# Performance work log

Measured on AMD Instinct MI355X. Metric: run time of the kernel, lower is better.

## Reference

```python
import jax, jax.numpy as jnp
import numpy as np

# Problem constants (from config / init_kwargs)
B = 32768          # batch_size
T = 20             # T_observation
N = 4              # N_agents
D = 8              # state_dim
H = 64             # gru_hidden_size


def setup_inputs() -> dict:
    key = jax.random.key(0)
    ks = jax.random.split(key, 6)
    s = lambda fan_in: 1.0 / np.sqrt(fan_in)
    return {
        "x": jax.random.normal(ks[0], (B, T * N * D), dtype=jnp.float32),
        # per-agent GRU weights: input proj (no bias), hidden proj (with bias); 3H = r|z|n
        "Wi": jax.random.normal(ks[1], (N, D, 3 * H), dtype=jnp.float32) * s(D),
        "Wh": jax.random.normal(ks[2], (N, H, 3 * H), dtype=jnp.float32) * s(H),
        "bh": jnp.zeros((N, 3 * H), dtype=jnp.float32),
        # MLP head: 256 -> 256 -> 128 -> 8
        "W0": jax.random.normal(ks[3], (N * H, 256), dtype=jnp.float32) * s(N * H),
        "b0": jnp.zeros((256,), dtype=jnp.float32),
        "W1": jax.random.normal(ks[4], (256, 128), dtype=jnp.float32) * s(256),
        "b1": jnp.zeros((128,), dtype=jnp.float32),
        "Wout": jax.random.normal(ks[5], (128, 8), dtype=jnp.float32) * s(128),
        "bout": jnp.zeros((8,), dtype=jnp.float32),
    }


def reference(x, Wi, Wh, bh, W0, b0, W1, b1, Wout, bout):
    b = x.shape[0]
    xr = x.reshape(b, T, N, D)
    # Precompute input-side gate projections for all agents/timesteps at once.
    xi = jnp.einsum("btnd,ndk->tbnk", xr, Wi)  # [T, B, N, 3H]

    def step(h, xi_t):
        # h: [B, N, H]; xi_t: [B, N, 3H]
        hg = jnp.einsum("bnh,nhk->bnk", h, Wh) + bh  # [B, N, 3H]
        ir, iz, inn = jnp.split(xi_t, 3, axis=-1)
        hr, hz, hn = jnp.split(hg, 3, axis=-1)
        r = jax.nn.sigmoid(ir + hr)
        z = jax.nn.sigmoid(iz + hz)
        n = jnp.tanh(inn + r * hn)
        h_new = (1.0 - z) * n + z * h  # flax GRUCell update
        return h_new, None

    h0 = jnp.zeros((b, N, H), dtype=x.dtype)
    hT, _ = jax.lax.scan(step, h0, xi)
    feat = hT.reshape(b, N * H)  # concat per-agent final hidden states

    h1 = jax.nn.relu(feat @ W0 + b0)
    h2 = jax.nn.relu(h1 @ W1 + b1)  # dropout deterministic -> identity
    goals = h2 @ Wout + bout
    return goals
```

## Files before the change

### kernel.cpp

```cpp
#include <hip/hip_runtime.h>
#include <math.h>

#define BT 32768
#define TT 20
#define NA 4
#define DD 8
#define HH 64

typedef _Float16 half8 __attribute__((ext_vector_type(8)));
typedef float f32x4 __attribute__((ext_vector_type(4)));
typedef unsigned short ushort;
typedef unsigned int uint;

#define SC1 -1.4426950408889634f
#define SC2 -2.8853900817779268f

__device__ __forceinline__ ushort f16b(float v) {
    _Float16 h = (_Float16)v;
    return *(ushort*)&h;
}
__device__ __forceinline__ void fsplit(float v, ushort& hi, ushort& lo) {
    _Float16 h = (_Float16)v;
    hi = *(ushort*)&h;
    float r = v - (float)h;
    _Float16 lw = (_Float16)r;
    lo = *(ushort*)&lw;
}

__global__ void prep_all(const float* __restrict__ Wh, const float* __restrict__ Wi,
                         const float* __restrict__ bh, const float* __restrict__ W0,
                         const float* __restrict__ W1, const float* __restrict__ Wout,
                         uint4* __restrict__ AG, uint4* __restrict__ W0F,
                         uint4* __restrict__ W1F, uint4* __restrict__ W2F) {
    const int gid = blockIdx.x * 256 + threadIdx.x;
    if (gid < 20480) {
        const int l = gid & 63;
        const int r2 = gid >> 6;
        const int fid = r2 % 20;
        const int jt = (r2 / 20) & 3;
        const int n = r2 / 80;
        const int s = fid & 1;
        const int gk = fid >> 1;
        int g, kq;
        if (gk < 9) { g = gk / 3; kq = gk % 3; } else { g = 3; kq = 2; }
        const int j = jt * 16 + (l & 15);
        const int lk = (l >> 4) & 3;
        const float scale = (g < 2) ? SC1 : SC2;
        uint wds[4];
        for (int i = 0; i < 4; ++i) {
            uint pk = 0;
            for (int hf = 0; hf < 2; ++hf) {
                const int e = 2 * i + hf;
                const int k = kq * 32 + 8 * lk + e;
                float v = 0.f;
                if (g < 3) {
                    if (k < 64)       v = Wh[(size_t)(n * 64 + k) * 192 + g * 64 + j];
                    else if (k < 72)  { if (g < 2) v = Wi[(size_t)(n * 8 + (k - 64)) * 192 + g * 64 + j]; }
                    else if (k == 72) v = bh[n * 192 + g * 64 + j];
                } else {
                    if (k >= 64 && k < 72) v = Wi[(size_t)(n * 8 + (k - 64)) * 192 + 128 + j];
                }
                v *= scale;
                ushort hi, lo; fsplit(v, hi, lo);
                pk |= ((uint)(s ? lo : hi)) << (16 * hf);
            }
            wds[i] = pk;
        }
        uint4 u; u.x = wds[0]; u.y = wds[1]; u.z = wds[2]; u.w = wds[3];
        AG[gid] = u;
    } else if (gid < 33024) {
        int id; const float* W; uint4* dst; int Nreal;
        if (gid < 28672)      { id = gid - 20480; W = W0;   dst = W0F; Nreal = 256; }
        else if (gid < 32768) { id = gid - 28672; W = W1;   dst = W1F; Nreal = 128; }
        else                  { id = gid - 32768; W = Wout; dst = W2F; Nreal = 8;   }
        const int l = id & 63;
        const int rr = id >> 6;
        const int kq = rr & 7;
        const int nt = rr >> 3;
        const int o = nt * 16 + (l & 15);
        const int lk = (l >> 4) & 3;
        const int ocols = (Nreal < 16) ? Nreal : ((Nreal + 15) & ~15);
        uint wds[4];
        for (int i = 0; i < 4; ++i) {
            uint pk = 0;
            for (int hf = 0; hf < 2; ++hf) {
                const int e = 2 * i + hf;
                const int k = kq * 32 + 8 * lk + e;
                float v = 0.f;
                if (o < Nreal) v = W[(size_t)k * Nreal + o];
                pk |= ((uint)f16b(v)) << (16 * hf);
            }
            wds[i] = pk;
        }
        uint4 u; u.x = wds[0]; u.y = wds[1]; u.z = wds[2]; u.w = wds[3];
        dst[id] = u;
        (void)ocols;
    }
}

__global__ __launch_bounds__(256, 2)
void gru_kernel(const float* __restrict__ x, const uint4* __restrict__ AG,
                ushort* __restrict__ featH, ushort* __restrict__ featL) {
    __shared__ __align__(16) ushort Bs[2][2][32 * 128];
    const int tid = threadIdx.x;
    const int l = tid & 63;
    const int w = tid >> 6;
    const int lrow = l & 15;
    const int lk = l >> 4;
    const int jt2 = w >> 1;
    const int nt = w & 1;
    const int n = blockIdx.y;
    const int bg = blockIdx.x * 32;

    {
        uint4 z = {0, 0, 0, 0};
        uint4* p = (uint4*)&Bs[0][0][0];
        for (int i = tid; i < 2048; i += 256) p[i] = z;
    }
    __syncthreads();

    half8 A[2][20];
#pragma unroll
    for (int jl = 0; jl < 2; ++jl) {
        const uint4* __restrict__ ab = AG + (size_t)((n * 4 + (jt2 * 2 + jl)) * 20) * 64 + l;
#pragma unroll
        for (int f = 0; f < 20; ++f) {
            uint4 v = ab[f * 64];
            A[jl][f] = *(half8*)&v;
        }
    }

    const int m0 = tid >> 3, d0 = tid & 7;
    const float* __restrict__ xp = x + (size_t)(bg + m0) * 640 + n * 8 + d0;

    {
        float v = xp[0];
        ushort hi, lo; fsplit(v, hi, lo);
        const int gsw = 8 ^ (m0 & 7);
        Bs[0][0][m0 * 128 + gsw * 8 + d0] = hi;
        Bs[0][1][m0 * 128 + gsw * 8 + d0] = lo;
    }
    if (tid < 64) {
        const int m = tid & 31, bu = tid >> 5;
        Bs[bu][0][m * 128 + (9 ^ (m & 7)) * 8 + 0] = 0x3C00;
    }
    __syncthreads();

    f32x4 hold[2];
#pragma unroll
    for (int jl = 0; jl < 2; ++jl)
#pragma unroll
        for (int r = 0; r < 4; ++r) hold[jl][r] = 0.f;

    const int rbase = (nt * 16 + lrow) * 128;
    const int key = lrow & 7;

    for (int t = 0; t < TT; ++t) {
        const int p = t & 1;
        float xnext = 0.f;
        if (t < TT - 1) xnext = xp[(t + 1) * 32];

        const ushort* __restrict__ BH = &Bs[p][0][0];
        const ushort* __restrict__ BL = &Bs[p][1][0];
        ushort* __restrict__ WH = &Bs[p ^ 1][0][0];
        ushort* __restrict__ WL = &Bs[p ^ 1][1][0];

        f32x4 acc[2][4];
#pragma unroll
        for (int jl = 0; jl < 2; ++jl)
#pragma unroll
            for (int g = 0; g < 4; ++g)
#pragma unroll
                for (int r = 0; r < 4; ++r) acc[jl][g][r] = 0.f;

#pragma unroll
        for (int kq = 0; kq < 3; ++kq) {
            const int gsw = (kq * 4 + lk) ^ key;
            const half8 bhf = *(const half8*)&BH[rbase + gsw * 8];
            const half8 blf = *(const half8*)&BL[rbase + gsw * 8];
#pragma unroll
            for (int jl = 0; jl < 2; ++jl) {
#pragma unroll
                for (int g = 0; g < 3; ++g) {
                    acc[jl][g] = __builtin_amdgcn_mfma_f32_16x16x32_f16(A[jl][(g * 3 + kq) * 2 + 0], bhf, acc[jl][g], 0, 0, 0);
                    acc[jl][g] = __builtin_amdgcn_mfma_f32_16x16x32_f16(A[jl][(g * 3 + kq) * 2 + 1], bhf, acc[jl][g], 0, 0, 0);
                    acc[jl][g] = __builtin_amdgcn_mfma_f32_16x16x32_f16(A[jl][(g * 3 + kq) * 2 + 0], blf, acc[jl][g], 0, 0, 0);
                }
                if (kq == 2) {
                    acc[jl][3] = __builtin_amdgcn_mfma_f32_16x16x32_f16(A[jl][18], bhf, acc[jl][3], 0, 0, 0);
                    acc[jl][3] = __builtin_amdgcn_mfma_f32_16x16x32_f16(A[jl][19], bhf, acc[jl][3], 0, 0, 0);
                    acc[jl][3] = __builtin_amdgcn_mfma_f32_16x16x32_f16(A[jl][18], blf, acc[jl][3], 0, 0, 0);
                }
            }
        }

#pragma unroll
        for (int jl = 0; jl < 2; ++jl) {
            float hv[4];
#pragma unroll
            for (int r = 0; r < 4; ++r) {
                const float rg = __builtin_amdgcn_rcpf(1.f + __builtin_amdgcn_exp2f(acc[jl][0][r]));
                const float zg = __builtin_amdgcn_rcpf(1.f + __builtin_amdgcn_exp2f(acc[jl][1][r]));
                const float sarg = fmaf(rg, acc[jl][2][r], acc[jl][3][r]);
                const float sg = __builtin_amdgcn_rcpf(1.f + __builtin_amdgcn_exp2f(sarg));
                const float ng = fmaf(2.f, sg, -1.f);
                hv[r] = fmaf(zg, hold[jl][r] - ng, ng);
                hold[jl][r] = hv[r];
            }
            if (t < TT - 1) {
                ushort hh[4], hl[4];
#pragma unroll
                for (int r = 0; r < 4; ++r) fsplit(hv[r], hh[r], hl[r]);
                const int jtg = jt2 * 2 + jl;
                const int gsw = (2 * jtg + (lk >> 1)) ^ key;
                const int off = rbase + gsw * 8 + 4 * (lk & 1);
                uint2 ph, pl;
                ph.x = (uint)hh[0] | ((uint)hh[1] << 16);
                ph.y = (uint)hh[2] | ((uint)hh[3] << 16);
                pl.x = (uint)hl[0] | ((uint)hl[1] << 16);
                pl.y = (uint)hl[2] | ((uint)hl[3] << 16);
                *(uint2*)&WH[off] = ph;
                *(uint2*)&WL[off] = pl;
            }
        }
        if (t < TT - 1) {
            ushort hi, lo; fsplit(xnext, hi, lo);
            const int gsw = 8 ^ (m0 & 7);
            WH[m0 * 128 + gsw * 8 + d0] = hi;
            WL[m0 * 128 + gsw * 8 + d0] = lo;
        }
        __syncthreads();
    }

#pragma unroll
    for (int jl = 0; jl < 2; ++jl) {
        ushort fh[4], fl[4];
#pragma unroll
        for (int r = 0; r < 4; ++r) fsplit(hold[jl][r], fh[r], fl[r]);
        uint2 ph, pl;
        ph.x = (uint)fh[0] | ((uint)fh[1] << 16);
        ph.y = (uint)fh[2] | ((uint)fh[3] << 16);
        pl.x = (uint)fl[0] | ((uint)fl[1] << 16);
        pl.y = (uint)fl[2] | ((uint)fl[3] << 16);
        const size_t fo = (size_t)(bg + nt * 16 + lrow) * 256 + n * 64 + (jt2 * 2 + jl) * 16 + 4 * lk;
        *(uint2*)&featH[fo] = ph;
        *(uint2*)&featL[fo] = pl;
    }
}

__global__ __launch_bounds__(256, 3)
void mlp_kernel(const ushort* __restrict__ featH, const ushort* __restrict__ featL,
                const uint4* __restrict__ W0F, const uint4* __restrict__ W1F,
                const uint4* __restrict__ W2F, const float* __restrict__ b0,
                const float* __restrict__ b1, const float* __restrict__ bout,
                float* __restrict__ out) {
    __shared__ __align__(16) ushort s1[2][32 * 256];
    __shared__ __align__(16) ushort s2[2][32 * 128];
    const int tid = threadIdx.x;
    const int l = tid & 63;
    const int w = tid >> 6;
    const int lrow = l & 15;
    const int lk = l >> 4;
    const int bg = blockIdx.x * 32;

    f32x4 a0[2][4];
#pragma unroll
    for (int bt = 0; bt < 2; ++bt)
#pragma unroll
        for (int q = 0; q < 4; ++q)
#pragma unroll
            for (int r = 0; r < 4; ++r) a0[bt][q][r] = 0.f;

#pragma unroll 2
    for (int kq = 0; kq < 8; ++kq) {
        half8 aH[2], aL[2];
#pragma unroll
        for (int bt = 0; bt < 2; ++bt) {
            const size_t off = (size_t)(bg + bt * 16 + lrow) * 256 + kq * 32 + 8 * lk;
            aH[bt] = *(const half8*)&featH[off];
            aL[bt] = *(const half8*)&featL[off];
        }
#pragma unroll
        for (int q = 0; q < 4; ++q) {
            const uint4 bv = W0F[((w * 4 + q) * 8 + kq) * 64 + l];
            const half8 bw = *(const half8*)&bv;
#pragma unroll
            for (int bt = 0; bt < 2; ++bt) {
                a0[bt][q] = __builtin_amdgcn_mfma_f32_16x16x32_f16(aH[bt], bw, a0[bt][q], 0, 0, 0);
                a0[bt][q] = __builtin_amdgcn_mfma_f32_16x16x32_f16(aL[bt], bw, a0[bt][q], 0, 0, 0);
            }
        }
    }
#pragma unroll
    for (int bt = 0; bt < 2; ++bt)
#pragma unroll
        for (int q = 0; q < 4; ++q) {
            const int nn = (w * 4 + q) * 16 + lrow;
            const float bias = b0[nn];
            const int gc = nn >> 3, sub = nn & 7;
#pragma unroll
            for (int r = 0; r < 4; ++r) {
                const int row = bt * 16 + 4 * lk + r;
                float v = a0[bt][q][r] + bias;
                v = v > 0.f ? v : 0.f;
                ushort hi, lo; fsplit(v, hi, lo);
                const int gsw = gc ^ (row & 7);
                s1[0][row * 256 + gsw * 8 + sub] = hi;
                s1[1][row * 256 + gsw * 8 + sub] = lo;
            }
        }
    __syncthreads();

    f32x4 a1[2][2];
#pragma unroll
    for (int bt = 0; bt < 2; ++bt)
#pragma unroll
        for (int u = 0; u < 2; ++u)
#pragma unroll
            for (int r = 0; r < 4; ++r) a1[bt][u][r] = 0.f;

#pragma unroll 2
    for (int kq = 0; kq < 8; ++kq) {
        half8 aH[2], aL[2];
#pragma unroll
        for (int bt = 0; bt < 2; ++bt) {
            const int row = bt * 16 + lrow;
            const int gsw = (kq * 4 + lk) ^ (row & 7);
            aH[bt] = *(const half8*)&s1[0][row * 256 + gsw * 8];
            aL[bt] = *(const half8*)&s1[1][row * 256 + gsw * 8];
        }
#pragma unroll
        for (int u = 0; u < 2; ++u) {
            const uint4 bv = W1F[((w + 4 * u) * 8 + kq) * 64 + l];
            const half8 bw = *(const half8*)&bv;
#pragma unroll
            for (int bt = 0; bt < 2; ++bt) {
                a1[bt][u] = __builtin_amdgcn_mfma_f32_16x16x32_f16(aH[bt], bw, a1[bt][u], 0, 0, 0);
                a1[bt][u] = __builtin_amdgcn_mfma_f32_16x16x32_f16(aL[bt], bw, a1[bt][u], 0, 0, 0);
            }
        }
    }
#pragma unroll
    for (int bt = 0; bt < 2; ++bt)
#pragma unroll
        for (int u = 0; u < 2; ++u) {
            const int nn = (w + 4 * u) * 16 + lrow;
            const float bias = b1[nn];
            const int gc = nn >> 3, sub = nn & 7;
#pragma unroll
            for (int r = 0; r < 4; ++r) {
                const int row = bt * 16 + 4 * lk + r;
                float v = a1[bt][u][r] + bias;
                v = v > 0.f ? v : 0.f;
                ushort hi, lo; fsplit(v, hi, lo);
                const int gsw = gc ^ (row & 7);
                s2[0][row * 128 + gsw * 8 + sub] = hi;
                s2[1][row * 128 + gsw * 8 + sub] = lo;
            }
        }
    __syncthreads();

    if (w < 2) {
        const int bt = w;
        f32x4 a2;
#pragma unroll
        for (int r = 0; r < 4; ++r) a2[r] = 0.f;
#pragma unroll
        for (int kq = 0; kq < 4; ++kq) {
            const int row = bt * 16 + lrow;
            const int gsw = (kq * 4 + lk) ^ (row & 7);
            const half8 aH = *(const half8*)&s2[0][row * 128 + gsw * 8];
            const half8 aL = *(const half8*)&s2[1][row * 128 + gsw * 8];
            const uint4 bv = W2F[kq * 64 + l];
            const half8 bw = *(const half8*)&bv;
            a2 = __builtin_amdgcn_mfma_f32_16x16x32_f16(aH, bw, a2, 0, 0, 0);
            a2 = __builtin_amdgcn_mfma_f32_16x16x32_f16(aL, bw, a2, 0, 0, 0);
        }
        if (lrow < 8) {
            const float bo = bout[lrow];
#pragma unroll
            for (int r = 0; r < 4; ++r)
                out[(size_t)(bg + bt * 16 + 4 * lk + r) * 8 + lrow] = a2[r] + bo;
        }
    }
}

extern "C" void kernel_launch(void* const* d_in, const int* in_sizes, int n_in,
                              void* d_out, int out_size, void* d_ws, size_t ws_size,
                              hipStream_t stream) {
    const float* x    = (const float*)d_in[0];
    const float* Wi   = (const float*)d_in[1];
    const float* Wh   = (const float*)d_in[2];
    const float* bh   = (const float*)d_in[3];
    const float* W0   = (const float*)d_in[4];
    const float* b0   = (const float*)d_in[5];
    const float* W1   = (const float*)d_in[6];
    const float* b1   = (const float*)d_in[7];
    const float* Wout = (const float*)d_in[8];
    const float* bout = (const float*)d_in[9];

    char* wsb = (char*)d_ws;
    ushort* featH = (ushort*)wsb;
    ushort* featL = (ushort*)(wsb + 16777216);
    uint4* AG  = (uint4*)(wsb + 33554432);
    uint4* W0F = (uint4*)(wsb + 33554432 + 327680);
    uint4* W1F = (uint4*)(wsb + 33554432 + 327680 + 131072);
    uint4* W2F = (uint4*)(wsb + 33554432 + 327680 + 131072 + 65536);

    prep_all<<<129, 256, 0, stream>>>(Wh, Wi, bh, W0, W1, Wout, AG, W0F, W1F, W2F);
    gru_kernel<<<dim3(BT / 32, NA), 256, 0, stream>>>(x, AG, featH, featL);
    mlp_kernel<<<BT / 32, 256, 0, stream>>>(featH, featL, W0F, W1F, W2F, b0, b1, bout, (float*)d_out);
}
```

Before: 378.6 us.

## Drop fp16 hi/lo split for GRU recurrence and remap warps to hidden tiles

```diff
diff --git a/kernel.cpp b/kernel.cpp
--- a/kernel.cpp
+++ b/kernel.cpp
@@ -79,7 +79,6 @@
         const int nt = rr >> 3;
         const int o = nt * 16 + (l & 15);
         const int lk = (l >> 4) & 3;
-        const int ocols = (Nreal < 16) ? Nreal : ((Nreal + 15) & ~15);
         uint wds[4];
         for (int i = 0; i < 4; ++i) {
             uint pk = 0;
@@ -94,155 +93,132 @@
         }
         uint4 u; u.x = wds[0]; u.y = wds[1]; u.z = wds[2]; u.w = wds[3];
         dst[id] = u;
-        (void)ocols;
-    }
-}
-
-__global__ __launch_bounds__(256, 2)
+    }
+}
+
+__global__ __launch_bounds__(256, 3)
 void gru_kernel(const float* __restrict__ x, const uint4* __restrict__ AG,
                 ushort* __restrict__ featH, ushort* __restrict__ featL) {
-    __shared__ __align__(16) ushort Bs[2][2][32 * 128];
+    __shared__ __align__(16) ushort Bs[2][32 * 128];
     const int tid = threadIdx.x;
     const int l = tid & 63;
     const int w = tid >> 6;
     const int lrow = l & 15;
     const int lk = l >> 4;
-    const int jt2 = w >> 1;
-    const int nt = w & 1;
     const int n = blockIdx.y;
     const int bg = blockIdx.x * 32;
 
     {
         uint4 z = {0, 0, 0, 0};
-        uint4* p = (uint4*)&Bs[0][0][0];
-        for (int i = tid; i < 2048; i += 256) p[i] = z;
+        uint4* p = (uint4*)&Bs[0][0];
+        for (int i = tid; i < 1024; i += 256) p[i] = z;
     }
     __syncthreads();
 
-    half8 A[2][20];
-#pragma unroll
-    for (int jl = 0; jl < 2; ++jl) {
-        const uint4* __restrict__ ab = AG + (size_t)((n * 4 + (jt2 * 2 + jl)) * 20) * 64 + l;
-#pragma unroll
-        for (int f = 0; f < 20; ++f) {
-            uint4 v = ab[f * 64];
-            A[jl][f] = *(half8*)&v;
-        }
-    }
-
-    const int m0 = tid >> 3, d0 = tid & 7;
-    const float* __restrict__ xp = x + (size_t)(bg + m0) * 640 + n * 8 + d0;
-
-    {
-        float v = xp[0];
-        ushort hi, lo; fsplit(v, hi, lo);
-        const int gsw = 8 ^ (m0 & 7);
-        Bs[0][0][m0 * 128 + gsw * 8 + d0] = hi;
-        Bs[0][1][m0 * 128 + gsw * 8 + d0] = lo;
+    half8 A[20];
+    const uint4* __restrict__ ab = AG + (size_t)((n * 4 + w) * 20) * 64 + l;
+#pragma unroll
+    for (int f = 0; f < 20; ++f) { uint4 v = ab[f * 64]; A[f] = *(half8*)&v; }
+
+    const int sm = tid >> 1, sh = tid & 1;
+    const float* __restrict__ xs = x + (size_t)(bg + sm) * 640 + n * 8 + sh * 4;
+
+    if (tid < 64) {
+        const float4 v = *(const float4*)xs;
+        uint2 pk;
+        pk.x = (uint)f16b(v.x) | ((uint)f16b(v.y) << 16);
+        pk.y = (uint)f16b(v.z) | ((uint)f16b(v.w) << 16);
+        *(uint2*)&Bs[0][sm * 128 + (8 ^ (sm & 7)) * 8 + sh * 4] = pk;
     }
     if (tid < 64) {
         const int m = tid & 31, bu = tid >> 5;
-        Bs[bu][0][m * 128 + (9 ^ (m & 7)) * 8 + 0] = 0x3C00;
+        Bs[bu][m * 128 + (9 ^ (m & 7)) * 8] = (ushort)0x3C00;
     }
     __syncthreads();
 
     f32x4 hold[2];
 #pragma unroll
-    for (int jl = 0; jl < 2; ++jl)
-#pragma unroll
-        for (int r = 0; r < 4; ++r) hold[jl][r] = 0.f;
-
-    const int rbase = (nt * 16 + lrow) * 128;
-    const int key = lrow & 7;
+    for (int nt = 0; nt < 2; ++nt)
+#pragma unroll
+        for (int r = 0; r < 4; ++r) hold[nt][r] = 0.f;
 
     for (int t = 0; t < TT; ++t) {
         const int p = t & 1;
-        float xnext = 0.f;
-        if (t < TT - 1) xnext = xp[(t + 1) * 32];
-
-        const ushort* __restrict__ BH = &Bs[p][0][0];
-        const ushort* __restrict__ BL = &Bs[p][1][0];
-        ushort* __restrict__ WH = &Bs[p ^ 1][0][0];
-        ushort* __restrict__ WL = &Bs[p ^ 1][1][0];
+        const ushort* __restrict__ BH = &Bs[p][0];
+        ushort* __restrict__ WH = &Bs[p ^ 1][0];
+
+        float4 xv = {0.f, 0.f, 0.f, 0.f};
+        if (tid < 64 && t < TT - 1) xv = *(const float4*)(xs + (t + 1) * 32);
 
         f32x4 acc[2][4];
 #pragma unroll
-        for (int jl = 0; jl < 2; ++jl)
+        for (int nt = 0; nt < 2; ++nt)
 #pragma unroll
             for (int g = 0; g < 4; ++g)
 #pragma unroll
-                for (int r = 0; r < 4; ++r) acc[jl][g][r] = 0.f;
-
-#pragma unroll
-        for (int kq = 0; kq < 3; ++kq) {
-            const int gsw = (kq * 4 + lk) ^ key;
-            const half8 bhf = *(const half8*)&BH[rbase + gsw * 8];
-            const half8 blf = *(const half8*)&BL[rbase + gsw * 8];
-#pragma unroll
-            for (int jl = 0; jl < 2; ++jl) {
+                for (int r = 0; r < 4; ++r) acc[nt][g][r] = 0.f;
+
+#pragma unroll
+        for (int nt = 0; nt < 2; ++nt) {
+            const int rbase = (nt * 16 + lrow) * 128;
+            const int key = lrow & 7;
+#pragma unroll
+            for (int kq = 0; kq < 3; ++kq) {
+                const half8 bf = *(const half8*)&BH[rbase + ((kq * 4 + lk) ^ key) * 8];
 #pragma unroll
                 for (int g = 0; g < 3; ++g) {
-                    acc[jl][g] = __builtin_amdgcn_mfma_f32_16x16x32_f16(A[jl][(g * 3 + kq) * 2 + 0], bhf, acc[jl][g], 0, 0, 0);
-                    acc[jl][g] = __builtin_amdgcn_mfma_f32_16x16x32_f16(A[jl][(g * 3 + kq) * 2 + 1], bhf, acc[jl][g], 0, 0, 0);
-                    acc[jl][g] = __builtin_amdgcn_mfma_f32_16x16x32_f16(A[jl][(g * 3 + kq) * 2 + 0], blf, acc[jl][g], 0, 0, 0);
+                    acc[nt][g] = __builtin_amdgcn_mfma_f32_16x16x32_f16(A[(g * 3 + kq) * 2 + 0], bf, acc[nt][g], 0, 0, 0);
+                    acc[nt][g] = __builtin_amdgcn_mfma_f32_16x16x32_f16(A[(g * 3 + kq) * 2 + 1], bf, acc[nt][g], 0, 0, 0);
                 }
                 if (kq == 2) {
-                    acc[jl][3] = __builtin_amdgcn_mfma_f32_16x16x32_f16(A[jl][18], bhf, acc[jl][3], 0, 0, 0);
-                    acc[jl][3] = __builtin_amdgcn_mfma_f32_16x16x32_f16(A[jl][19], bhf, acc[jl][3], 0, 0, 0);
-                    acc[jl][3] = __builtin_amdgcn_mfma_f32_16x16x32_f16(A[jl][18], blf, acc[jl][3], 0, 0, 0);
+                    acc[nt][3] = __builtin_amdgcn_mfma_f32_16x16x32_f16(A[18], bf, acc[nt][3], 0, 0, 0);
+                    acc[nt][3] = __builtin_amdgcn_mfma_f32_16x16x32_f16(A[19], bf, acc[nt][3], 0, 0, 0);
                 }
             }
         }
 
 #pragma unroll
-        for (int jl = 0; jl < 2; ++jl) {
-            float hv[4];
+        for (int nt = 0; nt < 2; ++nt) {
+            ushort hq[4];
 #pragma unroll
             for (int r = 0; r < 4; ++r) {
-                const float rg = __builtin_amdgcn_rcpf(1.f + __builtin_amdgcn_exp2f(acc[jl][0][r]));
-                const float zg = __builtin_amdgcn_rcpf(1.f + __builtin_amdgcn_exp2f(acc[jl][1][r]));
-                const float sarg = fmaf(rg, acc[jl][2][r], acc[jl][3][r]);
+                const float rg = __builtin_amdgcn_rcpf(1.f + __builtin_amdgcn_exp2f(acc[nt][0][r]));
+                const float zg = __builtin_amdgcn_rcpf(1.f + __builtin_amdgcn_exp2f(acc[nt][1][r]));
+                const float sarg = fmaf(rg, acc[nt][2][r], acc[nt][3][r]);
                 const float sg = __builtin_amdgcn_rcpf(1.f + __builtin_amdgcn_exp2f(sarg));
                 const float ng = fmaf(2.f, sg, -1.f);
-                hv[r] = fmaf(zg, hold[jl][r] - ng, ng);
-                hold[jl][r] = hv[r];
+                const float hv = fmaf(zg, hold[nt][r] - ng, ng);
+                hold[nt][r] = hv;
+                hq[r] = f16b(hv);
             }
             if (t < TT - 1) {
-                ushort hh[4], hl[4];
-#pragma unroll
-                for (int r = 0; r < 4; ++r) fsplit(hv[r], hh[r], hl[r]);
-                const int jtg = jt2 * 2 + jl;
-                const int gsw = (2 * jtg + (lk >> 1)) ^ key;
-                const int off = rbase + gsw * 8 + 4 * (lk & 1);
-                uint2 ph, pl;
-                ph.x = (uint)hh[0] | ((uint)hh[1] << 16);
-                ph.y = (uint)hh[2] | ((uint)hh[3] << 16);
-                pl.x = (uint)hl[0] | ((uint)hl[1] << 16);
-                pl.y = (uint)hl[2] | ((uint)hl[3] << 16);
-                *(uint2*)&WH[off] = ph;
-                *(uint2*)&WL[off] = pl;
-            }
-        }
-        if (t < TT - 1) {
-            ushort hi, lo; fsplit(xnext, hi, lo);
-            const int gsw = 8 ^ (m0 & 7);
-            WH[m0 * 128 + gsw * 8 + d0] = hi;
-            WL[m0 * 128 + gsw * 8 + d0] = lo;
+                const int gsw = (w * 2 + (lk >> 1)) ^ (lrow & 7);
+                uint2 pk;
+                pk.x = (uint)hq[0] | ((uint)hq[1] << 16);
+                pk.y = (uint)hq[2] | ((uint)hq[3] << 16);
+                *(uint2*)&WH[(nt * 16 + lrow) * 128 + gsw * 8 + 4 * (lk & 1)] = pk;
+            }
+        }
+        if (tid < 64 && t < TT - 1) {
+            uint2 pk;
+            pk.x = (uint)f16b(xv.x) | ((uint)f16b(xv.y) << 16);
+            pk.y = (uint)f16b(xv.z) | ((uint)f16b(xv.w) << 16);
+            *(uint2*)&WH[sm * 128 + (8 ^ (sm & 7)) * 8 + sh * 4] = pk;
         }
         __syncthreads();
     }
 
 #pragma unroll
-    for (int jl = 0; jl < 2; ++jl) {
+    for (int nt = 0; nt < 2; ++nt) {
         ushort fh[4], fl[4];
 #pragma unroll
-        for (int r = 0; r < 4; ++r) fsplit(hold[jl][r], fh[r], fl[r]);
+        for (int r = 0; r < 4; ++r) fsplit(hold[nt][r], fh[r], fl[r]);
         uint2 ph, pl;
         ph.x = (uint)fh[0] | ((uint)fh[1] << 16);
         ph.y = (uint)fh[2] | ((uint)fh[3] << 16);
         pl.x = (uint)fl[0] | ((uint)fl[1] << 16);
         pl.y = (uint)fl[2] | ((uint)fl[3] << 16);
-        const size_t fo = (size_t)(bg + nt * 16 + lrow) * 256 + n * 64 + (jt2 * 2 + jl) * 16 + 4 * lk;
+        const size_t fo = (size_t)(bg + nt * 16 + lrow) * 256 + n * 64 + w * 16 + 4 * lk;
         *(uint2*)&featH[fo] = ph;
         *(uint2*)&featL[fo] = pl;
     }
```

Measured after the change: 328.3 us. 13.3% less time.
